# Optimization experiments

Hardware: AMD Instinct MI355X
Metric: run time of the kernel (lower is better)

The kernel has to match this reference:

```python
import jax, jax.numpy as jnp
import numpy as np

B, E, H, W, L = 16, 32, 512, 512, 3  # batch, emb channels, height, width, n classes (bg/plant/disease)
MAX_NEIGHBOR = 3


def _per_image_loss(emb, pred, label, neighbor):
    """emb: (E,H,W) f32; pred: (L,H,W) f32 logits; label: (H,W) int32; neighbor: (L,MAX_NEIGHBOR) int32."""
    P = H * W
    emb_f = emb.reshape(E, P)                                      # (E,P)
    lab_f = label.reshape(P)
    onehot = (lab_f[None, :] == jnp.arange(L)[:, None]).astype(emb.dtype)  # (L,P)
    counts = onehot.sum(axis=1)                                    # (L,)

    # per-label mean embeddings (segment mean) and L2-normalized means (F.normalize eps=1e-12)
    means = (onehot @ emb_f.T) / counts[:, None]                   # (L,E)
    norm_means = means / jnp.maximum(jnp.linalg.norm(means, axis=1, keepdims=True), 1e-12)

    # intra loss: mean over masked pixels of (1 - cos(norm_mean, pixel)), labels 1..L-1
    pix_hat = emb_f / jnp.maximum(jnp.linalg.norm(emb_f, axis=0, keepdims=True), 1e-8)  # CosineSimilarity eps
    cos = norm_means @ pix_hat                                     # (L,P)
    intra_per = (onehot * (1.0 - cos)).sum(axis=1) / counts        # (L,)
    intra = intra_per[1:].sum() / (L - 1)

    # inter loss: pairwise cosine of normalized means, masked by neighbor table
    S = norm_means @ norm_means.T                                  # (L,L)
    # inter_mask: for main_label>=1, mark neighbor entries until first 0 (break semantics)
    valid = jnp.cumprod((neighbor != 0).astype(jnp.float32), axis=1)        # (L,MAX_NEIGHBOR)
    rows = jnp.broadcast_to(jnp.arange(L)[:, None], (L, MAX_NEIGHBOR))
    row_ok = (rows >= 1).astype(jnp.float32)
    mask = jnp.zeros((L, L), dtype=jnp.float32).at[
        rows.reshape(-1), neighbor.reshape(-1)
    ].max((valid * row_ok).reshape(-1))
    inter = (S * mask).sum() / mask.sum()

    # cross-entropy (labels in [0,L), ignore_index=255 never hit here), mean over pixels
    logp = jax.nn.log_softmax(pred, axis=0)                        # (L,H,W)
    ce = -jnp.take_along_axis(logp, label[None, :, :].astype(jnp.int32), axis=0).mean()

    return intra + inter + ce


def setup_inputs() -> dict:
    key = jax.random.key(0)
    k1, k2, k3 = jax.random.split(key, 3)
    embedding = jax.random.normal(k1, (B, E, H, W), dtype=jnp.float32)
    prediction = jax.random.normal(k2, (B, L, H, W), dtype=jnp.float32)
    class_label = jax.random.randint(k3, (B, H, W), 0, L).astype(jnp.int32)
    # realistic neighbor table: plant(1)<->disease(2) adjacent, 0 = terminator
    nb = np.tile(np.array([[0, 0, 0], [2, 0, 0], [1, 0, 0]], dtype=np.int32), (B, 1, 1))
    neighbor = jnp.asarray(nb)
    return {"embedding": embedding, "prediction": prediction,
            "class_label": class_label, "neighbor": neighbor}


def reference(embedding, prediction, class_label, neighbor):
    losses = jax.vmap(_per_image_loss)(embedding, prediction, class_label, neighbor)  # (B,)
    return losses.sum()
```

## Files before the change

### kernel.cpp

```cpp
#include <hip/hip_runtime.h>
#include <math.h>

#define BATCH 16
#define EMB   32
#define HW    262144
#define NL    3

#define BLOCKS_PER_IMG 128
#define PX_PER_BLOCK  (HW / BLOCKS_PER_IMG)
#define TILE_PX       128
#define N_ITERS       (PX_PER_BLOCK / TILE_PX)

#define WS_COUNTS 0
#define WS_SE     64
#define WS_SH     (WS_SE + BATCH*96)
#define WS_CE     (WS_SH + BATCH*96)
#define WS_FLOATS (WS_CE + 1)

__global__ __launch_bounds__(256) void accum_kernel(
        const float* __restrict__ emb, const int* __restrict__ label,
        float* __restrict__ ws)
{
    const int tid = threadIdx.x;
    const int ps  = tid & 31;
    const int eg  = tid >> 5;
    const int wv  = tid >> 6;
    const bool lowHalf = (tid & 63) < 32;
    const int b   = blockIdx.x / BLOCKS_PER_IMG;
    const int blk = blockIdx.x % BLOCKS_PER_IMG;

    const float* embB = emb + (size_t)b * EMB * HW;
    const int*   labB = label + (size_t)b * HW;
    const size_t pixBase = (size_t)blk * PX_PER_BLOCK;

    __shared__ float4 part[4][32];

    float accE[NL][4] = {};
    float accH[NL][4] = {};
    float cnt[NL] = {0.f, 0.f, 0.f};

    for (int it = 0; it < N_ITERS; ++it) {
        const size_t p = pixBase + (size_t)it * TILE_PX + (size_t)ps * 4;
        const float4 v0 = *(const float4*)(embB + (size_t)(eg*4+0)*HW + p);
        const float4 v1 = *(const float4*)(embB + (size_t)(eg*4+1)*HW + p);
        const float4 v2 = *(const float4*)(embB + (size_t)(eg*4+2)*HW + p);
        const float4 v3 = *(const float4*)(embB + (size_t)(eg*4+2)*HW + p - 2*HW + 3*HW);
        const float4 v3r = *(const float4*)(embB + (size_t)(eg*4+3)*HW + p);
        const int4 lab  = *(const int4*)(labB + p);
        const float4 V3 = v3r; (void)v3;

        float4 s;
        s.x = v0.x*v0.x + v1.x*v1.x + v2.x*v2.x + V3.x*V3.x;
        s.y = v0.y*v0.y + v1.y*v1.y + v2.y*v2.y + V3.y*V3.y;
        s.z = v0.z*v0.z + v1.z*v1.z + v2.z*v2.z + V3.z*V3.z;
        s.w = v0.w*v0.w + v1.w*v1.w + v2.w*v2.w + V3.w*V3.w;
        s.x += __shfl_xor(s.x, 32);
        s.y += __shfl_xor(s.y, 32);
        s.z += __shfl_xor(s.z, 32);
        s.w += __shfl_xor(s.w, 32);
        if (lowHalf) part[wv][ps] = s;
        __syncthreads();
        const float4 t0 = part[0][ps], t1 = part[1][ps],
                     t2 = part[2][ps], t3 = part[3][ps];
        float invn[4];
        invn[0] = 1.0f / fmaxf(sqrtf(t0.x + t1.x + t2.x + t3.x), 1e-8f);
        invn[1] = 1.0f / fmaxf(sqrtf(t0.y + t1.y + t2.y + t3.y), 1e-8f);
        invn[2] = 1.0f / fmaxf(sqrtf(t0.z + t1.z + t2.z + t3.z), 1e-8f);
        invn[3] = 1.0f / fmaxf(sqrtf(t0.w + t1.w + t2.w + t3.w), 1e-8f);
        __syncthreads();

        const float chv[4][4] = {
            {v0.x, v1.x, v2.x, V3.x},
            {v0.y, v1.y, v2.y, V3.y},
            {v0.z, v1.z, v2.z, V3.z},
            {v0.w, v1.w, v2.w, V3.w}};
        const int labs[4] = {lab.x, lab.y, lab.z, lab.w};

        #pragma unroll
        for (int j = 0; j < 4; ++j) {
            const float m0 = (labs[j] == 0) ? 1.f : 0.f;
            const float m1 = (labs[j] == 1) ? 1.f : 0.f;
            const float m2 = (labs[j] == 2) ? 1.f : 0.f;
            const float iv = invn[j];
            if (eg == 0) { cnt[0] += m0; cnt[1] += m1; cnt[2] += m2; }
            #pragma unroll
            for (int k = 0; k < 4; ++k) {
                const float v  = chv[j][k];
                const float vh = v * iv;
                accE[0][k] = fmaf(m0, v,  accE[0][k]);
                accE[1][k] = fmaf(m1, v,  accE[1][k]);
                accE[2][k] = fmaf(m2, v,  accE[2][k]);
                accH[0][k] = fmaf(m0, vh, accH[0][k]);
                accH[1][k] = fmaf(m1, vh, accH[1][k]);
                accH[2][k] = fmaf(m2, vh, accH[2][k]);
            }
        }
    }

    #pragma unroll
    for (int o = 16; o >= 1; o >>= 1) {
        #pragma unroll
        for (int l = 0; l < NL; ++l) {
            #pragma unroll
            for (int k = 0; k < 4; ++k) {
                accE[l][k] += __shfl_xor(accE[l][k], o);
                accH[l][k] += __shfl_xor(accH[l][k], o);
            }
            cnt[l] += __shfl_xor(cnt[l], o);
        }
    }
    if (ps == 0) {
        float* se = ws + WS_SE + b * 96;
        float* sh = ws + WS_SH + b * 96;
        #pragma unroll
        for (int l = 0; l < NL; ++l) {
            #pragma unroll
            for (int k = 0; k < 4; ++k) {
                atomicAdd(&se[l*32 + eg*4 + k], accE[l][k]);
                atomicAdd(&sh[l*32 + eg*4 + k], accH[l][k]);
            }
        }
        if (eg == 0) {
            atomicAdd(&ws[WS_COUNTS + b*4 + 0], cnt[0]);
            atomicAdd(&ws[WS_COUNTS + b*4 + 1], cnt[1]);
            atomicAdd(&ws[WS_COUNTS + b*4 + 2], cnt[2]);
        }
    }
}

__device__ __forceinline__ float ce1(float a, float b, float c, int l) {
    const float m = fmaxf(fmaxf(a, b), c);
    const float s = __expf(a - m) + __expf(b - m) + __expf(c - m);
    const float zl = (l == 0) ? a : ((l == 1) ? b : c);
    return m + __logf(s) - zl;
}

__global__ __launch_bounds__(256) void ce_kernel(
        const float* __restrict__ pred, const int* __restrict__ label,
        float* __restrict__ ws)
{
    const long P4 = HW / 4;
    const long nq = (long)BATCH * P4;
    float local = 0.f;
    for (long q = (long)blockIdx.x * blockDim.x + threadIdx.x; q < nq;
         q += (long)gridDim.x * blockDim.x) {
        const int b  = (int)(q / P4);
        const long p = (q % P4) * 4;
        const float* pb = pred + (size_t)b * 3 * HW;
        const float4 z0 = *(const float4*)(pb + p);
        const float4 z1 = *(const float4*)(pb + HW + p);
        const float4 z2 = *(const float4*)(pb + 2 * HW + p);
        const int4 lab  = *(const int4*)(label + (size_t)b * HW + p);
        local += ce1(z0.x, z1.x, z2.x, lab.x);
        local += ce1(z0.y, z1.y, z2.y, lab.y);
        local += ce1(z0.z, z1.z, z2.z, lab.z);
        local += ce1(z0.w, z1.w, z2.w, lab.w);
    }
    #pragma unroll
    for (int o = 32; o >= 1; o >>= 1) local += __shfl_xor(local, o);
    __shared__ float wsum[4];
    if ((threadIdx.x & 63) == 0) wsum[threadIdx.x >> 6] = local;
    __syncthreads();
    if (threadIdx.x == 0) {
        const float t = wsum[0] + wsum[1] + wsum[2] + wsum[3];
        atomicAdd(&ws[WS_CE], t * (1.0f / (float)HW));
    }
}

__global__ __launch_bounds__(512) void final_kernel(
        const int* __restrict__ nbr, const float* __restrict__ ws,
        float* __restrict__ out)
{
    const int tid = threadIdx.x;
    const int b = tid >> 5;
    const int e = tid & 31;
    __shared__ float total;
    if (tid == 0) total = 0.f;
    __syncthreads();

    const float* se = ws + WS_SE + b * 96;
    const float* sh = ws + WS_SH + b * 96;
    const float c0 = ws[WS_COUNTS + b*4 + 0];
    const float c1 = ws[WS_COUNTS + b*4 + 1];
    const float c2 = ws[WS_COUNTS + b*4 + 2];

    float mean0 = se[0*32 + e] / c0;
    float mean1 = se[1*32 + e] / c1;
    float mean2 = se[2*32 + e] / c2;

    float n0 = mean0*mean0, n1 = mean1*mean1, n2 = mean2*mean2;
    #pragma unroll
    for (int o = 16; o >= 1; o >>= 1) {
        n0 += __shfl_xor(n0, o);
        n1 += __shfl_xor(n1, o);
        n2 += __shfl_xor(n2, o);
    }
    const float nm0 = mean0 / fmaxf(sqrtf(n0), 1e-12f);
    const float nm1 = mean1 / fmaxf(sqrtf(n1), 1e-12f);
    const float nm2 = mean2 / fmaxf(sqrtf(n2), 1e-12f);

    float d1  = nm1 * sh[1*32 + e];
    float d2  = nm2 * sh[2*32 + e];
    float s10 = nm1 * nm0, s11 = nm1 * nm1, s12 = nm1 * nm2;
    float s20 = nm2 * nm0, s21 = nm2 * nm1, s22 = nm2 * nm2;
    #pragma unroll
    for (int o = 16; o >= 1; o >>= 1) {
        d1  += __shfl_xor(d1, o);  d2  += __shfl_xor(d2, o);
        s10 += __shfl_xor(s10, o); s11 += __shfl_xor(s11, o); s12 += __shfl_xor(s12, o);
        s20 += __shfl_xor(s20, o); s21 += __shfl_xor(s21, o); s22 += __shfl_xor(s22, o);
    }

    if (e == 0) {
        float S[3][3];
        S[1][0] = s10; S[1][1] = s11; S[1][2] = s12;
        S[2][0] = s20; S[2][1] = s21; S[2][2] = s22;
        S[0][0] = S[0][1] = S[0][2] = 0.f;
        float mask[3][3] = {{0.f,0.f,0.f},{0.f,0.f,0.f},{0.f,0.f,0.f}};
        for (int row = 1; row < 3; ++row) {
            int prod = 1;
            for (int j = 0; j < 3; ++j) {
                const int v = nbr[b*9 + row*3 + j];
                if (v == 0) prod = 0;
                if (prod) mask[row][v] = 1.f;
            }
        }
        float num = 0.f, den = 0.f;
        for (int row = 1; row < 3; ++row)
            for (int col = 0; col < 3; ++col) {
                num += S[row][col] * mask[row][col];
                den += mask[row][col];
            }
        const float inter = num / den;
        const float ip1 = 1.f - d1 / c1;
        const float ip2 = 1.f - d2 / c2;
        const float loss = 0.5f * (ip1 + ip2) + inter;
        atomicAdd(&total, loss);
    }
    __syncthreads();
    if (tid == 0) out[0] = total + ws[WS_CE];
}

extern "C" void kernel_launch(void* const* d_in, const int* in_sizes, int n_in,
                              void* d_out, int out_size, void* d_ws, size_t ws_size,
                              hipStream_t stream) {
    const float* emb   = (const float*)d_in[0];
    const float* pred  = (const float*)d_in[1];
    const int*   label = (const int*)d_in[2];
    const int*   nbr   = (const int*)d_in[3];
    float* ws  = (float*)d_ws;
    float* out = (float*)d_out;

    hipMemsetAsync(d_ws, 0, WS_FLOATS * sizeof(float), stream);
    accum_kernel<<<BATCH * BLOCKS_PER_IMG, 256, 0, stream>>>(emb, label, ws);
    ce_kernel<<<2048, 256, 0, stream>>>(pred, label, ws);
    final_kernel<<<1, 512, 0, stream>>>(nbr, ws, out);
}
```

Before: 796.3 us.

## Fuse cross-entropy into accumulation kernel with register prefetch and double-buffered shared partials

Merges the separate cross-entropy pass into the embedding accumulation kernel, so labels are read once and one launch is removed. Each tile's CE work is assigned round-robin to one of the eight channel-group slices. The loop also prefetches the next tile's embedding and labels into registers. It double-buffers the shared norm partials so the second barrier per iteration can be dropped. The cost is more registers per thread, extra atomics on the CE accumulator, and uneven work across warps on CE iterations.

```diff
diff --git a/kernel.cpp b/kernel.cpp
--- a/kernel.cpp
+++ b/kernel.cpp
@@ -17,9 +17,16 @@
 #define WS_CE     (WS_SH + BATCH*96)
 #define WS_FLOATS (WS_CE + 1)
 
-__global__ __launch_bounds__(256) void accum_kernel(
-        const float* __restrict__ emb, const int* __restrict__ label,
-        float* __restrict__ ws)
+__device__ __forceinline__ float ce1(float a, float b, float c, int l) {
+    const float m = fmaxf(fmaxf(a, b), c);
+    const float s = __expf(a - m) + __expf(b - m) + __expf(c - m);
+    const float zl = (l == 0) ? a : ((l == 1) ? b : c);
+    return m + __logf(s) - zl;
+}
+
+__global__ __launch_bounds__(256) void fused_kernel(
+        const float* __restrict__ emb, const float* __restrict__ pred,
+        const int* __restrict__ label, float* __restrict__ ws)
 {
     const int tid = threadIdx.x;
     const int ps  = tid & 31;
@@ -29,51 +36,73 @@
     const int b   = blockIdx.x / BLOCKS_PER_IMG;
     const int blk = blockIdx.x % BLOCKS_PER_IMG;
 
-    const float* embB = emb + (size_t)b * EMB * HW;
-    const int*   labB = label + (size_t)b * HW;
+    const float* embB  = emb  + (size_t)b * EMB * HW;
+    const float* predB = pred + (size_t)b * 3 * HW;
+    const int*   labB  = label + (size_t)b * HW;
     const size_t pixBase = (size_t)blk * PX_PER_BLOCK;
 
-    __shared__ float4 part[4][32];
+    const float* ch0 = embB + (size_t)(eg*4+0)*HW;
+    const float* ch1 = embB + (size_t)(eg*4+1)*HW;
+    const float* ch2 = embB + (size_t)(eg*4+2)*HW;
+    const float* ch3 = embB + (size_t)(eg*4+3)*HW;
+
+    __shared__ float4 part[2][4][32];
 
     float accE[NL][4] = {};
     float accH[NL][4] = {};
     float cnt[NL] = {0.f, 0.f, 0.f};
+    float ce = 0.f;
+
+    size_t p = pixBase + (size_t)ps * 4;
+    float4 v0 = *(const float4*)(ch0 + p);
+    float4 v1 = *(const float4*)(ch1 + p);
+    float4 v2 = *(const float4*)(ch2 + p);
+    float4 v3 = *(const float4*)(ch3 + p);
+    int4  lab = *(const int4*)(labB + p);
 
     for (int it = 0; it < N_ITERS; ++it) {
-        const size_t p = pixBase + (size_t)it * TILE_PX + (size_t)ps * 4;
-        const float4 v0 = *(const float4*)(embB + (size_t)(eg*4+0)*HW + p);
-        const float4 v1 = *(const float4*)(embB + (size_t)(eg*4+1)*HW + p);
-        const float4 v2 = *(const float4*)(embB + (size_t)(eg*4+2)*HW + p);
-        const float4 v3 = *(const float4*)(embB + (size_t)(eg*4+2)*HW + p - 2*HW + 3*HW);
-        const float4 v3r = *(const float4*)(embB + (size_t)(eg*4+3)*HW + p);
-        const int4 lab  = *(const int4*)(labB + p);
-        const float4 V3 = v3r; (void)v3;
+        const size_t pn = (it + 1 < N_ITERS) ? (p + TILE_PX)
+                                             : (pixBase + (size_t)ps * 4);
+        const float4 n0 = *(const float4*)(ch0 + pn);
+        const float4 n1 = *(const float4*)(ch1 + pn);
+        const float4 n2 = *(const float4*)(ch2 + pn);
+        const float4 n3 = *(const float4*)(ch3 + pn);
+        const int4 nlab = *(const int4*)(labB + pn);
+
+        const bool doCE = (eg == (it & 7));
+        float4 z0, z1, z2;
+        if (doCE) {
+            z0 = *(const float4*)(predB + p);
+            z1 = *(const float4*)(predB + HW + p);
+            z2 = *(const float4*)(predB + 2*HW + p);
+        }
 
         float4 s;
-        s.x = v0.x*v0.x + v1.x*v1.x + v2.x*v2.x + V3.x*V3.x;
-        s.y = v0.y*v0.y + v1.y*v1.y + v2.y*v2.y + V3.y*V3.y;
-        s.z = v0.z*v0.z + v1.z*v1.z + v2.z*v2.z + V3.z*V3.z;
-        s.w = v0.w*v0.w + v1.w*v1.w + v2.w*v2.w + V3.w*V3.w;
+        s.x = v0.x*v0.x + v1.x*v1.x + v2.x*v2.x + v3.x*v3.x;
+        s.y = v0.y*v0.y + v1.y*v1.y + v2.y*v2.y + v3.y*v3.y;
+        s.z = v0.z*v0.z + v1.z*v1.z + v2.z*v2.z + v3.z*v3.z;
+        s.w = v0.w*v0.w + v1.w*v1.w + v2.w*v2.w + v3.w*v3.w;
         s.x += __shfl_xor(s.x, 32);
         s.y += __shfl_xor(s.y, 32);
         s.z += __shfl_xor(s.z, 32);
         s.w += __shfl_xor(s.w, 32);
-        if (lowHalf) part[wv][ps] = s;
+        if (lowHalf) part[it & 1][wv][ps] = s;
         __syncthreads();
-        const float4 t0 = part[0][ps], t1 = part[1][ps],
-                     t2 = part[2][ps], t3 = part[3][ps];
+        const float4 t0 = part[it & 1][0][ps];
+        const float4 t1 = part[it & 1][1][ps];
+        const float4 t2 = part[it & 1][2][ps];
+        const float4 t3 = part[it & 1][3][ps];
         float invn[4];
         invn[0] = 1.0f / fmaxf(sqrtf(t0.x + t1.x + t2.x + t3.x), 1e-8f);
         invn[1] = 1.0f / fmaxf(sqrtf(t0.y + t1.y + t2.y + t3.y), 1e-8f);
         invn[2] = 1.0f / fmaxf(sqrtf(t0.z + t1.z + t2.z + t3.z), 1e-8f);
         invn[3] = 1.0f / fmaxf(sqrtf(t0.w + t1.w + t2.w + t3.w), 1e-8f);
-        __syncthreads();
 
         const float chv[4][4] = {
-            {v0.x, v1.x, v2.x, V3.x},
-            {v0.y, v1.y, v2.y, V3.y},
-            {v0.z, v1.z, v2.z, V3.z},
-            {v0.w, v1.w, v2.w, V3.w}};
+            {v0.x, v1.x, v2.x, v3.x},
+            {v0.y, v1.y, v2.y, v3.y},
+            {v0.z, v1.z, v2.z, v3.z},
+            {v0.w, v1.w, v2.w, v3.w}};
         const int labs[4] = {lab.x, lab.y, lab.z, lab.w};
 
         #pragma unroll
@@ -95,6 +124,15 @@
                 accH[2][k] = fmaf(m2, vh, accH[2][k]);
             }
         }
+
+        if (doCE) {
+            ce += ce1(z0.x, z1.x, z2.x, labs[0]);
+            ce += ce1(z0.y, z1.y, z2.y, labs[1]);
+            ce += ce1(z0.z, z1.z, z2.z, labs[2]);
+            ce += ce1(z0.w, z1.w, z2.w, labs[3]);
+        }
+
+        v0 = n0; v1 = n1; v2 = n2; v3 = n3; lab = nlab; p = pn;
     }
 
     #pragma unroll
@@ -108,6 +146,7 @@
             }
             cnt[l] += __shfl_xor(cnt[l], o);
         }
+        ce += __shfl_xor(ce, o);
     }
     if (ps == 0) {
         float* se = ws + WS_SE + b * 96;
@@ -120,50 +159,12 @@
                 atomicAdd(&sh[l*32 + eg*4 + k], accH[l][k]);
             }
         }
+        atomicAdd(&ws[WS_CE], ce * (1.0f / (float)HW));
         if (eg == 0) {
             atomicAdd(&ws[WS_COUNTS + b*4 + 0], cnt[0]);
             atomicAdd(&ws[WS_COUNTS + b*4 + 1], cnt[1]);
             atomicAdd(&ws[WS_COUNTS + b*4 + 2], cnt[2]);
         }
-    }
-}
-
-__device__ __forceinline__ float ce1(float a, float b, float c, int l) {
-    const float m = fmaxf(fmaxf(a, b), c);
-    const float s = __expf(a - m) + __expf(b - m) + __expf(c - m);
-    const float zl = (l == 0) ? a : ((l == 1) ? b : c);
-    return m + __logf(s) - zl;
-}
-
-__global__ __launch_bounds__(256) void ce_kernel(
-        const float* __restrict__ pred, const int* __restrict__ label,
-        float* __restrict__ ws)
-{
-    const long P4 = HW / 4;
-    const long nq = (long)BATCH * P4;
-    float local = 0.f;
-    for (long q = (long)blockIdx.x * blockDim.x + threadIdx.x; q < nq;
-         q += (long)gridDim.x * blockDim.x) {
-        const int b  = (int)(q / P4);
-        const long p = (q % P4) * 4;
-        const float* pb = pred + (size_t)b * 3 * HW;
-        const float4 z0 = *(const float4*)(pb + p);
-        const float4 z1 = *(const float4*)(pb + HW + p);
-        const float4 z2 = *(const float4*)(pb + 2 * HW + p);
-        const int4 lab  = *(const int4*)(label + (size_t)b * HW + p);
-        local += ce1(z0.x, z1.x, z2.x, lab.x);
-        local += ce1(z0.y, z1.y, z2.y, lab.y);
-        local += ce1(z0.z, z1.z, z2.z, lab.z);
-        local += ce1(z0.w, z1.w, z2.w, lab.w);
-    }
-    #pragma unroll
-    for (int o = 32; o >= 1; o >>= 1) local += __shfl_xor(local, o);
-    __shared__ float wsum[4];
-    if ((threadIdx.x & 63) == 0) wsum[threadIdx.x >> 6] = local;
-    __syncthreads();
-    if (threadIdx.x == 0) {
-        const float t = wsum[0] + wsum[1] + wsum[2] + wsum[3];
-        atomicAdd(&ws[WS_CE], t * (1.0f / (float)HW));
     }
 }
 
@@ -251,7 +252,6 @@
     float* out = (float*)d_out;
 
     hipMemsetAsync(d_ws, 0, WS_FLOATS * sizeof(float), stream);
-    accum_kernel<<<BATCH * BLOCKS_PER_IMG, 256, 0, stream>>>(emb, label, ws);
-    ce_kernel<<<2048, 256, 0, stream>>>(pred, label, ws);
+    fused_kernel<<<BATCH * BLOCKS_PER_IMG, 256, 0, stream>>>(emb, pred, label, ws);
     final_kernel<<<1, 512, 0, stream>>>(nbr, ws, out);
 }
```

New measurement: 768.7 us. 3.5% less time.
